# Kernel optimization log

Measured on AMD Instinct MI355X. Metric: run time of the kernel, lower is better.

Reference implementation:

```python
import jax, jax.numpy as jnp
import numpy as np

B, L, D, H = 2, 2048, 2048, 16
HD = D // H  # 128, must be even for RoPE


def rope(x, seq_len, theta=10000.0):
    """Apply RoPE to x of shape [B, H, L, Dh]."""
    d = x.shape[-1]
    freqs = 1.0 / theta ** (jnp.arange(0, d, 2, dtype=x.dtype) / d)  # [d/2]
    t = jnp.arange(seq_len, dtype=x.dtype)
    f = jnp.outer(t, freqs)                      # [L, d/2]
    sin = jnp.repeat(jnp.sin(f), 2, axis=-1)     # [L, d]
    cos = jnp.repeat(jnp.cos(f), 2, axis=-1)
    x1, x2 = x[..., ::2], x[..., 1::2]
    x_rot = jnp.stack([-x2, x1], axis=-1).reshape(x.shape)
    return x * cos + x_rot * sin


def setup_inputs() -> dict:
    key = jax.random.key(0)
    k1, k2, k3 = jax.random.split(key, 3)
    x = jax.random.normal(k1, (B, L, D), dtype=jnp.float32)
    w_qkv = jax.random.normal(k2, (D, 3 * D), dtype=jnp.float32) * (1.0 / np.sqrt(D))
    w_proj = jax.random.normal(k3, (D, D), dtype=jnp.float32) * (1.0 / np.sqrt(D))
    return {"x": x, "w_qkv": w_qkv, "w_proj": w_proj}


def reference(x, w_qkv, w_proj):
    Bc, Lc, Dc = x.shape
    scale = 1.0 / np.sqrt(HD)
    qkv = (x @ w_qkv).reshape(Bc, Lc, 3, H, HD)
    q, k, v = qkv[:, :, 0], qkv[:, :, 1], qkv[:, :, 2]   # [B, L, H, Dh]
    # transpose to [B, H, L, Dh], then RoPE (position axis = L)
    q = rope(jnp.transpose(q, (0, 2, 1, 3)), Lc)
    k = rope(jnp.transpose(k, (0, 2, 1, 3)), Lc)
    v = jnp.transpose(v, (0, 2, 1, 3))
    att = jnp.einsum("bhqd,bhkd->bhqk", q, k) * scale   # [B, H, L, L]
    att = jax.nn.softmax(att, axis=-1)
    out = jnp.einsum("bhqk,bhkd->bhqd", att, v)          # [B, H, L, Dh]
    out = jnp.transpose(out, (0, 2, 1, 3)).reshape(Bc, Lc, Dc)
    return out @ w_proj
```

## Files before the change

### kernel.cpp

```cpp
#include <hip/hip_runtime.h>
#include <hip/hip_bf16.h>
#include <cstdint>

typedef short short8 __attribute__((ext_vector_type(8)));
typedef float f32x4 __attribute__((ext_vector_type(4)));
typedef int i32x4 __attribute__((ext_vector_type(4)));

#define AS1 __attribute__((address_space(1)))
#define AS3 __attribute__((address_space(3)))

static __device__ __forceinline__ void async_cp16(const void* g, void* l) {
  __builtin_amdgcn_global_load_lds((const AS1 unsigned int*)g, (AS3 unsigned int*)l, 16, 0, 0);
}

static __device__ __forceinline__ ushort f2bf(float f) {
  unsigned u = __builtin_bit_cast(unsigned, f);
  u += 0x7fffu + ((u >> 16) & 1u);
  return (ushort)(u >> 16);
}
static __device__ __forceinline__ float bf2f(ushort h) {
  unsigned u = ((unsigned)h) << 16;
  return __builtin_bit_cast(float, u);
}

#define FENCE asm volatile("" ::: "memory")
#define BARRIER do { FENCE; __builtin_amdgcn_s_barrier(); FENCE; } while (0)
#define WAITLGKM asm volatile("s_waitcnt lgkmcnt(0)" ::: "memory")
#define WAITVM(N) asm volatile("s_waitcnt vmcnt(" #N ")" ::: "memory")

__global__ void cvt_bf16_kernel(const float* __restrict__ in, ushort* __restrict__ out, int n4) {
  int i = blockIdx.x * blockDim.x + threadIdx.x;
  if (i >= n4) return;
  float4 v = ((const float4*)in)[i];
  ushort4 o;
  o.x = f2bf(v.x); o.y = f2bf(v.y); o.z = f2bf(v.z); o.w = f2bf(v.w);
  ((ushort4*)out)[i] = o;
}

__global__ void transpose_cvt_kernel(const float* __restrict__ in, ushort* __restrict__ out,
                                     int R, int C) {
  __shared__ ushort tile[32][33];
  int c0 = blockIdx.x * 32, r0 = blockIdx.y * 32;
  int tx = threadIdx.x, ty = threadIdx.y;
  for (int j = 0; j < 32; j += 8)
    tile[ty + j][tx] = f2bf(in[(size_t)(r0 + ty + j) * C + c0 + tx]);
  __syncthreads();
  for (int j = 0; j < 32; j += 8)
    out[(size_t)(c0 + ty + j) * R + r0 + tx] = tile[tx][ty + j];
}

__global__ void rope_tab_kernel(float2* __restrict__ tab) {
  int idx = blockIdx.x * 256 + threadIdx.x;
  int i = idx & 63, l = idx >> 6;
  float inv = __builtin_amdgcn_exp2f(-(float)i * (13.287712379549449f / 64.0f));
  float f = (float)l * inv;
  float s, c;
  sincosf(f, &s, &c);
  tab[idx] = make_float2(c, s);
}

__global__ __launch_bounds__(512, 2) void gemm_qkv_kernel(
    const ushort* __restrict__ A, const ushort* __restrict__ Bt,
    ushort* __restrict__ qr, ushort* __restrict__ kr, ushort* __restrict__ vt,
    const float2* __restrict__ rtab, int K, int N) {
  __shared__ __align__(16) ushort smem[65536];
  const int tid = threadIdx.x;
  const int wave = tid >> 6, lane = tid & 63;
  const int wm = wave >> 2, wn = wave & 3;
  const int m0 = blockIdx.y * 256, n0 = blockIdx.x * 256;
  const int frl = lane & 15, fq = lane >> 4;
  const int sx = fq ^ (frl & 7);
  const int srow = tid >> 3;
  const int slog8 = (((tid & 7) ^ ((tid >> 3) & 7)) << 3);

  const ushort* aG = A + (size_t)(m0 + srow) * K + slog8;
  const ushort* bG = Bt + (size_t)(n0 + srow) * K + slog8;
  ushort* lw = smem + wave * 512;

  f32x4 acc[8][4] = {};
  short8 aF[4][2], bF[2][2][2];

  auto stA = [&](int tt, int h) {
    ushort* l = lw + (tt & 1) * 32768 + h * 8192;
    const ushort* g = aG + (size_t)(h * 128) * K + tt * 64;
    async_cp16(g, l);
    async_cp16(g + (size_t)64 * K, l + 4096);
  };
  auto stB = [&](int tt, int h) {
    ushort* l = lw + (tt & 1) * 32768 + 16384 + h * 8192;
    const ushort* g = bG + (size_t)(h * 128) * K + tt * 64;
    async_cp16(g, l);
    async_cp16(g + (size_t)64 * K, l + 4096);
  };
  auto LDA = [&](int buf, int mh) {
#pragma unroll
    for (int mf = 0; mf < 4; ++mf)
#pragma unroll
      for (int kk = 0; kk < 2; ++kk)
        aF[mf][kk] = *(const short8*)(smem + buf * 32768 +
            (wm * 128 + mh * 64 + mf * 16 + frl) * 64 + ((sx ^ (kk << 2)) << 3));
  };
  auto LDB = [&](int buf, int nh) {
#pragma unroll
    for (int j = 0; j < 2; ++j)
#pragma unroll
      for (int kk = 0; kk < 2; ++kk)
        bF[nh][j][kk] = *(const short8*)(smem + buf * 32768 + 16384 +
            (wn * 64 + nh * 32 + j * 16 + frl) * 64 + ((sx ^ (kk << 2)) << 3));
  };
  auto MFMAQ = [&](int mh, int nh) {
    __builtin_amdgcn_s_setprio(1);
#pragma unroll
    for (int mf = 0; mf < 4; ++mf)
#pragma unroll
      for (int j = 0; j < 2; ++j)
#pragma unroll
        for (int kk = 0; kk < 2; ++kk)
          acc[mh * 4 + mf][nh * 2 + j] = __builtin_amdgcn_mfma_f32_16x16x32_bf16(
              aF[mf][kk], bF[nh][j][kk], acc[mh * 4 + mf][nh * 2 + j], 0, 0, 0);
    __builtin_amdgcn_s_setprio(0);
  };

  stB(0, 0); stB(0, 1); stA(0, 0); stA(0, 1);
  stB(1, 0); stB(1, 1);
  WAITVM(4);
  BARRIER;

  const int NT = K >> 6;
  for (int i = 0; i < NT / 2 - 1; ++i) {
    const int t = 2 * i;
    LDA(0, 0); LDB(0, 0); stA(t + 1, 0);
    BARRIER; WAITLGKM; MFMAQ(0, 0); BARRIER;
    LDB(0, 1); stA(t + 1, 1);
    BARRIER; WAITLGKM; MFMAQ(0, 1); BARRIER;
    LDA(0, 1); stB(t + 2, 0);
    BARRIER; WAITLGKM; MFMAQ(1, 0); BARRIER;
    stB(t + 2, 1);
    BARRIER; WAITLGKM; MFMAQ(1, 1); WAITVM(4); BARRIER;
    LDA(1, 0); LDB(1, 0); stA(t + 2, 0);
    BARRIER; WAITLGKM; MFMAQ(0, 0); BARRIER;
    LDB(1, 1); stA(t + 2, 1);
    BARRIER; WAITLGKM; MFMAQ(0, 1); BARRIER;
    LDA(1, 1); stB(t + 3, 0);
    BARRIER; WAITLGKM; MFMAQ(1, 0); BARRIER;
    stB(t + 3, 1);
    BARRIER; WAITLGKM; MFMAQ(1, 1); WAITVM(4); BARRIER;
  }
  {
    const int t = NT - 2;
    LDA(0, 0); LDB(0, 0); stA(t + 1, 0);
    BARRIER; WAITLGKM; MFMAQ(0, 0); BARRIER;
    LDB(0, 1); stA(t + 1, 1);
    BARRIER; WAITLGKM; MFMAQ(0, 1); BARRIER;
    LDA(0, 1);
    BARRIER; WAITLGKM; MFMAQ(1, 0); BARRIER;
    BARRIER; WAITLGKM; MFMAQ(1, 1); WAITVM(0); BARRIER;
    LDA(1, 0); LDB(1, 0);
    BARRIER; WAITLGKM; MFMAQ(0, 0); BARRIER;
    LDB(1, 1);
    BARRIER; WAITLGKM; MFMAQ(0, 1); BARRIER;
    LDA(1, 1);
    BARRIER; WAITLGKM; MFMAQ(1, 0); BARRIER;
    BARRIER; WAITLGKM; MFMAQ(1, 1); BARRIER;
  }

  const int rq = fq * 4;
  if (n0 < 4096) {
    ushort* dst = (n0 >= 2048) ? kr : qr;
#pragma unroll
    for (int mi = 0; mi < 8; ++mi)
#pragma unroll
      for (int ni = 0; ni < 4; ++ni) {
        int col = n0 + wn * 64 + ni * 16 + frl;
        int rem = col & 2047, h = rem >> 7, dh = rem & 127;
        int ip = dh >> 1;
        float sgn = (dh & 1) ? 1.0f : -1.0f;
#pragma unroll
        for (int r = 0; r < 4; ++r) {
          int row = m0 + wm * 128 + mi * 16 + rq + r;
          int b = row >> 11, l = row & 2047;
          float v = acc[mi][ni][r];
          float vp = __shfl_xor(v, 1);
          float2 cs2 = rtab[l * 64 + ip];
          float o = v * cs2.x + sgn * vp * cs2.y;
          dst[((size_t)((b << 4) + h) * 2048 + l) * 128 + dh] = f2bf(o);
        }
      }
  } else {
    ushort* vtile = smem + wave * 1024;
    const int col0 = n0 + wn * 64;
    const int row0 = m0 + wm * 128;
    const int b = row0 >> 11, l0 = row0 & 2047;
    const int swz = (frl & 3) << 4;
#pragma unroll
    for (int hm = 0; hm < 2; ++hm)
#pragma unroll
      for (int ni = 0; ni < 4; ++ni) {
#pragma unroll
        for (int mi = 0; mi < 4; ++mi)
#pragma unroll
          for (int r = 0; r < 4; ++r) {
            int ll = mi * 16 + rq + r;
            vtile[frl * 64 + (ll ^ swz)] = f2bf(acc[hm * 4 + mi][ni][r]);
          }
#pragma unroll
        for (int tt = 0; tt < 2; ++tt) {
          int dl = tt * 8 + (lane >> 3);
          int l8 = (lane & 7) * 8;
          int lsw = l8 ^ ((dl & 3) << 4);
          int rem = (col0 + ni * 16 + dl) & 2047;
          int h = rem >> 7, dh = rem & 127;
          *(short8*)(vt + ((size_t)((b << 4) + h) * 128 + dh) * 2048 + l0 + hm * 64 + l8) =
              *(const short8*)(vtile + dl * 64 + lsw);
        }
      }
  }
}

__global__ __launch_bounds__(256) void gemm_out_kernel(
    const ushort* __restrict__ A, const ushort* __restrict__ Bt,
    float* __restrict__ C, int K, int N) {
  __shared__ __align__(16) ushort As[128 * 32];
  __shared__ __align__(16) ushort Bs[128 * 32];
  const int tid = threadIdx.x;
  const int wave = tid >> 6, lane = tid & 63;
  const int wr = (wave >> 1) * 64, wc = (wave & 1) * 64;
  const int m0 = blockIdx.y * 128, n0 = blockIdx.x * 128;
  const int l4 = lane >> 2, lb8 = (lane & 3) * 8;
  const int fr = lane & 15, fq8 = (lane >> 4) * 8;

  f32x4 acc[4][4] = {};

  for (int k0 = 0; k0 < K; k0 += 32) {
#pragma unroll
    for (int j = 0; j < 2; ++j) {
      const int r = wave * 32 + j * 16 + l4;
      async_cp16(A + (size_t)(m0 + r) * K + k0 + lb8, As + wave * 1024 + j * 512);
      async_cp16(Bt + (size_t)(n0 + r) * K + k0 + lb8, Bs + wave * 1024 + j * 512);
    }
    __syncthreads();
    short8 af[4], bf_[4];
#pragma unroll
    for (int i = 0; i < 4; ++i) {
      af[i] = *(const short8*)(As + (wr + i * 16 + fr) * 32 + fq8);
      bf_[i] = *(const short8*)(Bs + (wc + i * 16 + fr) * 32 + fq8);
    }
#pragma unroll
    for (int mi = 0; mi < 4; ++mi)
#pragma unroll
      for (int ni = 0; ni < 4; ++ni)
        acc[mi][ni] = __builtin_amdgcn_mfma_f32_16x16x32_bf16(af[mi], bf_[ni], acc[mi][ni], 0, 0, 0);
    __syncthreads();
  }

  const int rq = (lane >> 4) * 4;
#pragma unroll
  for (int mi = 0; mi < 4; ++mi)
#pragma unroll
    for (int ni = 0; ni < 4; ++ni) {
      int col = n0 + wc + ni * 16 + fr;
#pragma unroll
      for (int r = 0; r < 4; ++r) {
        int row = m0 + wr + mi * 16 + rq + r;
        C[(size_t)row * N + col] = acc[mi][ni][r];
      }
    }
}

__global__ __launch_bounds__(512, 4) void flash_kernel(
    const ushort* __restrict__ qr, const ushort* __restrict__ kr,
    const ushort* __restrict__ vtg, ushort* __restrict__ att) {
  __shared__ __align__(16) ushort KV[2][16384];

  const int tid = threadIdx.x;
  const int wave = tid >> 6, lane = tid & 63;
  const int bid = blockIdx.x;
  const int swzb = (bid & 7) * 64 + (bid >> 3);
  const int qt = swzb & 15;
  const int bh = swzb >> 4;
  const int q0 = qt * 128 + wave * 16;
  const size_t bh_base = (size_t)bh * 2048 * 128;

  const int fr = lane & 15, fq = lane >> 4;
  const float cs = 0.08838834764831845f * 1.4426950408889634f;
  const int kswz = (fr & 7) << 3;

  const int krow0 = wave * 8 + fq;
  const int kgc = fr * 8;
  const int vrow0 = wave * 16 + (lane >> 3);
  const int vgc = (lane & 7) * 8;

  auto stage = [&](int kt, int buf) {
#pragma unroll
    for (int i = 0; i < 2; ++i) {
      const int krow = krow0 + i * 4;
      async_cp16(kr + bh_base + (size_t)(kt * 64 + krow) * 128 + (kgc ^ ((krow & 7) << 3)),
                 &KV[buf][(wave * 2 + i) * 512]);
      const int vrow = vrow0 + i * 8;
      async_cp16(vtg + bh_base + (size_t)vrow * 2048 + kt * 64 + (vgc ^ ((vrow & 7) << 3)),
                 &KV[buf][8192 + (wave * 2 + i) * 512]);
    }
  };

  short8 qf[4];
  {
    const ushort* qp = qr + bh_base + (size_t)(q0 + fr) * 128 + fq * 8;
#pragma unroll
    for (int kc = 0; kc < 4; ++kc) qf[kc] = *(const short8*)(qp + kc * 32);
  }

  f32x4 oacc[8];
#pragma unroll
  for (int i = 0; i < 8; ++i) oacc[i] = (f32x4){0.f, 0.f, 0.f, 0.f};
  float l_lane = 0.f;

  const int LA = fr + 32 * (fq & 1);
  const bool hi = fq >= 2;

  stage(0, 0);
  stage(1, 1);
  WAITVM(4);
  BARRIER;

#pragma unroll 2
  for (int kt = 0; kt < 32; ++kt) {
    const int bo = (kt & 1) * 16384;
    const ushort* kv = &KV[0][0];

    f32x4 sv[4];
    __builtin_amdgcn_s_setprio(1);
#pragma unroll
    for (int nt = 0; nt < 4; ++nt) {
      f32x4 a = (f32x4){0.f, 0.f, 0.f, 0.f};
#pragma unroll
      for (int kc = 0; kc < 4; ++kc) {
        short8 kf = *(const short8*)(kv + bo + (nt * 16 + fr) * 128 + ((kc * 32 + fq * 8) ^ kswz));
        a = __builtin_amdgcn_mfma_f32_16x16x32_bf16(kf, qf[kc], a, 0, 0, 0);
      }
      sv[nt] = a;
    }
    __builtin_amdgcn_s_setprio(0);

    int dA[4], dB[4];
#pragma unroll
    for (int nt = 0; nt < 4; ++nt) {
      float p0 = __builtin_amdgcn_exp2f(sv[nt][0] * cs);
      float p1 = __builtin_amdgcn_exp2f(sv[nt][1] * cs);
      float p2 = __builtin_amdgcn_exp2f(sv[nt][2] * cs);
      float p3 = __builtin_amdgcn_exp2f(sv[nt][3] * cs);
      l_lane += (p0 + p1) + (p2 + p3);
      dA[nt] = (int)f2bf(p0) | ((int)f2bf(p1) << 16);
      dB[nt] = (int)f2bf(p2) | ((int)f2bf(p3) << 16);
    }

    __builtin_amdgcn_s_setprio(1);
#pragma unroll
    for (int kc2 = 0; kc2 < 2; ++kc2) {
      const int ntE = 2 * kc2, ntO = 2 * kc2 + 1;
      int e0 = __shfl(dA[ntE], LA), e1 = __shfl(dB[ntE], LA);
      int e2 = __shfl(dA[ntE], LA + 16), e3 = __shfl(dB[ntE], LA + 16);
      int o0 = __shfl(dA[ntO], LA), o1 = __shfl(dB[ntO], LA);
      int o2 = __shfl(dA[ntO], LA + 16), o3 = __shfl(dB[ntO], LA + 16);
      i32x4 w = (i32x4){hi ? o0 : e0, hi ? o1 : e1, hi ? o2 : e2, hi ? o3 : e3};
      short8 pa = __builtin_bit_cast(short8, w);
#pragma unroll
      for (int dt = 0; dt < 8; ++dt) {
        short8 vf = *(const short8*)(kv + bo + 8192 + (dt * 16 + fr) * 64 +
                                     ((kc2 * 32 + fq * 8) ^ kswz));
        oacc[dt] = __builtin_amdgcn_mfma_f32_16x16x32_bf16(pa, vf, oacc[dt], 0, 0, 0);
      }
    }
    __builtin_amdgcn_s_setprio(0);

    BARRIER;
    if (kt < 30) {
      stage(kt + 2, kt & 1);
      WAITVM(4);
    } else {
      WAITVM(0);
    }
    BARRIER;
  }

  l_lane += __shfl_xor(l_lane, 16);
  l_lane += __shfl_xor(l_lane, 32);
  const int b = bh >> 4, h = bh & 15;
#pragma unroll
  for (int r = 0; r < 4; ++r) {
    float inv = 1.0f / __shfl(l_lane, fq * 4 + r);
    size_t row = (size_t)(b * 2048 + q0 + fq * 4 + r) * 2048 + h * 128;
#pragma unroll
    for (int dt = 0; dt < 8; ++dt)
      att[row + dt * 16 + fr] = f2bf(oacc[dt][r] * inv);
  }
}

extern "C" void kernel_launch(void* const* d_in, const int* in_sizes, int n_in,
                              void* d_out, int out_size, void* d_ws, size_t ws_size,
                              hipStream_t stream) {
  const float* x = (const float*)d_in[0];
  const float* w_qkv = (const float*)d_in[1];
  const float* w_proj = (const float*)d_in[2];
  float* out = (float*)d_out;

  char* p = (char*)d_ws;
  ushort* xb = (ushort*)p;  p += (size_t)4096 * 2048 * 2;
  ushort* wqt = (ushort*)p; p += (size_t)6144 * 2048 * 2;
  ushort* wpt = (ushort*)p; p += (size_t)2048 * 2048 * 2;
  ushort* qr = (ushort*)p;  p += (size_t)32 * 2048 * 128 * 2;
  ushort* kr = (ushort*)p;  p += (size_t)32 * 2048 * 128 * 2;
  ushort* vt = (ushort*)p;  p += (size_t)32 * 2048 * 128 * 2;
  ushort* att = (ushort*)p; p += (size_t)4096 * 2048 * 2;
  float2* rtab = (float2*)p; p += (size_t)2048 * 64 * 8;

  rope_tab_kernel<<<512, 256, 0, stream>>>(rtab);
  cvt_bf16_kernel<<<8192, 256, 0, stream>>>(x, xb, 4096 * 2048 / 4);
  transpose_cvt_kernel<<<dim3(192, 64), dim3(32, 8), 0, stream>>>(w_qkv, wqt, 2048, 6144);
  transpose_cvt_kernel<<<dim3(64, 64), dim3(32, 8), 0, stream>>>(w_proj, wpt, 2048, 2048);
  gemm_qkv_kernel<<<dim3(24, 16), 512, 0, stream>>>(xb, wqt, qr, kr, vt, rtab, 2048, 6144);
  flash_kernel<<<512, 512, 0, stream>>>(qr, kr, vt, att);
  gemm_out_kernel<<<dim3(16, 32), 256, 0, stream>>>(att, wpt, out, 2048, 2048);
}
```

Baseline: 420.9 us.

## Switch flash attention to 32x32x16 MFMA with 32 query rows per wave

Rewrites the flash attention kernel so each wave handles 32 query rows using 32x32x16 bf16 MFMAs instead of 16 rows with 16x16x32. The block tile grows to 256 queries, which halves the grid and the number of times each block's K/V tiles are streamed from global memory. The P-matrix repacking becomes a single cross-half xor shuffle, and the row-sum reduction and output store are remapped to the 32x32 accumulator layout. In exchange, register pressure rises (launch bounds drop to 2 blocks per CU) and only 256 blocks are launched, which may leave some CUs underfilled.

```diff
diff --git a/kernel.cpp b/kernel.cpp
--- a/kernel.cpp
+++ b/kernel.cpp
@@ -4,6 +4,7 @@
 
 typedef short short8 __attribute__((ext_vector_type(8)));
 typedef float f32x4 __attribute__((ext_vector_type(4)));
+typedef float f32x16 __attribute__((ext_vector_type(16)));
 typedef int i32x4 __attribute__((ext_vector_type(4)));
 
 #define AS1 __attribute__((address_space(1)))
@@ -267,7 +268,7 @@
     }
 }
 
-__global__ __launch_bounds__(512, 4) void flash_kernel(
+__global__ __launch_bounds__(512, 2) void flash_kernel(
     const ushort* __restrict__ qr, const ushort* __restrict__ kr,
     const ushort* __restrict__ vtg, ushort* __restrict__ att) {
   __shared__ __align__(16) ushort KV[2][16384];
@@ -275,18 +276,18 @@
   const int tid = threadIdx.x;
   const int wave = tid >> 6, lane = tid & 63;
   const int bid = blockIdx.x;
-  const int swzb = (bid & 7) * 64 + (bid >> 3);
-  const int qt = swzb & 15;
-  const int bh = swzb >> 4;
-  const int q0 = qt * 128 + wave * 16;
+  const int swzb = (bid & 7) * 32 + (bid >> 3);
+  const int qt = swzb & 7;
+  const int bh = swzb >> 3;
+  const int q0 = qt * 256 + wave * 32;
   const size_t bh_base = (size_t)bh * 2048 * 128;
 
-  const int fr = lane & 15, fq = lane >> 4;
+  const int qi = lane & 31, hi = lane >> 5;
   const float cs = 0.08838834764831845f * 1.4426950408889634f;
-  const int kswz = (fr & 7) << 3;
-
-  const int krow0 = wave * 8 + fq;
-  const int kgc = fr * 8;
+  const int rsw = (qi & 7) << 3;
+
+  const int krow0 = wave * 8 + (lane >> 4);
+  const int kgc = (lane & 15) * 8;
   const int vrow0 = wave * 16 + (lane >> 3);
   const int vgc = (lane & 7) * 8;
 
@@ -302,20 +303,19 @@
     }
   };
 
-  short8 qf[4];
+  short8 qf[8];
   {
-    const ushort* qp = qr + bh_base + (size_t)(q0 + fr) * 128 + fq * 8;
-#pragma unroll
-    for (int kc = 0; kc < 4; ++kc) qf[kc] = *(const short8*)(qp + kc * 32);
-  }
-
-  f32x4 oacc[8];
-#pragma unroll
-  for (int i = 0; i < 8; ++i) oacc[i] = (f32x4){0.f, 0.f, 0.f, 0.f};
+    const ushort* qp = qr + bh_base + (size_t)(q0 + qi) * 128 + hi * 8;
+#pragma unroll
+    for (int c = 0; c < 8; ++c) qf[c] = *(const short8*)(qp + c * 16);
+  }
+
+  f32x16 oacc[4];
+#pragma unroll
+  for (int nt = 0; nt < 4; ++nt)
+#pragma unroll
+    for (int r = 0; r < 16; ++r) oacc[nt][r] = 0.f;
   float l_lane = 0.f;
-
-  const int LA = fr + 32 * (fq & 1);
-  const bool hi = fq >= 2;
 
   stage(0, 0);
   stage(1, 1);
@@ -327,47 +327,53 @@
     const int bo = (kt & 1) * 16384;
     const ushort* kv = &KV[0][0];
 
-    f32x4 sv[4];
+    f32x16 s0, s1;
+#pragma unroll
+    for (int r = 0; r < 16; ++r) { s0[r] = 0.f; s1[r] = 0.f; }
+    const ushort* kp0 = kv + bo + (size_t)(0 * 32 + qi) * 128;
+    const ushort* kp1 = kv + bo + (size_t)(1 * 32 + qi) * 128;
     __builtin_amdgcn_s_setprio(1);
 #pragma unroll
-    for (int nt = 0; nt < 4; ++nt) {
-      f32x4 a = (f32x4){0.f, 0.f, 0.f, 0.f};
-#pragma unroll
-      for (int kc = 0; kc < 4; ++kc) {
-        short8 kf = *(const short8*)(kv + bo + (nt * 16 + fr) * 128 + ((kc * 32 + fq * 8) ^ kswz));
-        a = __builtin_amdgcn_mfma_f32_16x16x32_bf16(kf, qf[kc], a, 0, 0, 0);
-      }
-      sv[nt] = a;
+    for (int c = 0; c < 8; ++c) {
+      const int co = (c * 16 + hi * 8) ^ rsw;
+      short8 kf0 = *(const short8*)(kp0 + co);
+      short8 kf1 = *(const short8*)(kp1 + co);
+      s0 = __builtin_amdgcn_mfma_f32_32x32x16_bf16(kf0, qf[c], s0, 0, 0, 0);
+      s1 = __builtin_amdgcn_mfma_f32_32x32x16_bf16(kf1, qf[c], s1, 0, 0, 0);
     }
     __builtin_amdgcn_s_setprio(0);
 
-    int dA[4], dB[4];
-#pragma unroll
-    for (int nt = 0; nt < 4; ++nt) {
-      float p0 = __builtin_amdgcn_exp2f(sv[nt][0] * cs);
-      float p1 = __builtin_amdgcn_exp2f(sv[nt][1] * cs);
-      float p2 = __builtin_amdgcn_exp2f(sv[nt][2] * cs);
-      float p3 = __builtin_amdgcn_exp2f(sv[nt][3] * cs);
-      l_lane += (p0 + p1) + (p2 + p3);
-      dA[nt] = (int)f2bf(p0) | ((int)f2bf(p1) << 16);
-      dB[nt] = (int)f2bf(p2) | ((int)f2bf(p3) << 16);
+    int pk[2][8];
+#pragma unroll
+    for (int m = 0; m < 8; ++m) {
+      float a0 = __builtin_amdgcn_exp2f(s0[2 * m] * cs);
+      float a1 = __builtin_amdgcn_exp2f(s0[2 * m + 1] * cs);
+      float b0 = __builtin_amdgcn_exp2f(s1[2 * m] * cs);
+      float b1 = __builtin_amdgcn_exp2f(s1[2 * m + 1] * cs);
+      l_lane += (a0 + a1) + (b0 + b1);
+      pk[0][m] = (int)f2bf(a0) | ((int)f2bf(a1) << 16);
+      pk[1][m] = (int)f2bf(b0) | ((int)f2bf(b1) << 16);
     }
 
     __builtin_amdgcn_s_setprio(1);
 #pragma unroll
-    for (int kc2 = 0; kc2 < 2; ++kc2) {
-      const int ntE = 2 * kc2, ntO = 2 * kc2 + 1;
-      int e0 = __shfl(dA[ntE], LA), e1 = __shfl(dB[ntE], LA);
-      int e2 = __shfl(dA[ntE], LA + 16), e3 = __shfl(dB[ntE], LA + 16);
-      int o0 = __shfl(dA[ntO], LA), o1 = __shfl(dB[ntO], LA);
-      int o2 = __shfl(dA[ntO], LA + 16), o3 = __shfl(dB[ntO], LA + 16);
-      i32x4 w = (i32x4){hi ? o0 : e0, hi ? o1 : e1, hi ? o2 : e2, hi ? o3 : e3};
+    for (int ks = 0; ks < 4; ++ks) {
+      const int kb = ks >> 1, s2 = ks & 1;
+      const int a0 = pk[kb][4 * s2 + 0], a1 = pk[kb][4 * s2 + 1];
+      const int a2 = pk[kb][4 * s2 + 2], a3 = pk[kb][4 * s2 + 3];
+      const int p0 = __shfl_xor(a0, 32), p1 = __shfl_xor(a1, 32);
+      const int p2 = __shfl_xor(a2, 32), p3 = __shfl_xor(a3, 32);
+      i32x4 w;
+      w[0] = hi ? p2 : a0;
+      w[1] = hi ? p3 : a1;
+      w[2] = hi ? a2 : p0;
+      w[3] = hi ? a3 : p1;
       short8 pa = __builtin_bit_cast(short8, w);
-#pragma unroll
-      for (int dt = 0; dt < 8; ++dt) {
-        short8 vf = *(const short8*)(kv + bo + 8192 + (dt * 16 + fr) * 64 +
-                                     ((kc2 * 32 + fq * 8) ^ kswz));
-        oacc[dt] = __builtin_amdgcn_mfma_f32_16x16x32_bf16(pa, vf, oacc[dt], 0, 0, 0);
+      const int vco = (ks * 16 + hi * 8) ^ rsw;
+#pragma unroll
+      for (int nt = 0; nt < 4; ++nt) {
+        short8 vf = *(const short8*)(kv + bo + 8192 + (size_t)(nt * 32 + qi) * 64 + vco);
+        oacc[nt] = __builtin_amdgcn_mfma_f32_32x32x16_bf16(pa, vf, oacc[nt], 0, 0, 0);
       }
     }
     __builtin_amdgcn_s_setprio(0);
@@ -382,16 +388,17 @@
     BARRIER;
   }
 
-  l_lane += __shfl_xor(l_lane, 16);
   l_lane += __shfl_xor(l_lane, 32);
+  const float linv = 1.0f / l_lane;
   const int b = bh >> 4, h = bh & 15;
 #pragma unroll
-  for (int r = 0; r < 4; ++r) {
-    float inv = 1.0f / __shfl(l_lane, fq * 4 + r);
-    size_t row = (size_t)(b * 2048 + q0 + fq * 4 + r) * 2048 + h * 128;
-#pragma unroll
-    for (int dt = 0; dt < 8; ++dt)
-      att[row + dt * 16 + fr] = f2bf(oacc[dt][r] * inv);
+  for (int r = 0; r < 16; ++r) {
+    const int crow = (r & 3) + 8 * (r >> 2) + 4 * hi;
+    const float inv = __shfl(linv, crow);
+    const size_t rowa = (size_t)(b * 2048 + q0 + crow) * 2048 + h * 128;
+#pragma unroll
+    for (int nt = 0; nt < 4; ++nt)
+      att[rowa + nt * 32 + qi] = f2bf(oacc[nt][r] * inv);
   }
 }
 
@@ -418,6 +425,6 @@
   transpose_cvt_kernel<<<dim3(192, 64), dim3(32, 8), 0, stream>>>(w_qkv, wqt, 2048, 6144);
   transpose_cvt_kernel<<<dim3(64, 64), dim3(32, 8), 0, stream>>>(w_proj, wpt, 2048, 2048);
   gemm_qkv_kernel<<<dim3(24, 16), 512, 0, stream>>>(xb, wqt, qr, kr, vt, rtab, 2048, 6144);
-  flash_kernel<<<512, 512, 0, stream>>>(qr, kr, vt, att);
+  flash_kernel<<<256, 512, 0, stream>>>(qr, kr, vt, att);
   gemm_out_kernel<<<dim3(16, 32), 256, 0, stream>>>(att, wpt, out, 2048, 2048);
 }
```

Result: faster. 403.5 us (-4.1%).
